# Kernel tuning notes

Measured on AMD Instinct MI355X. Metric: run time of the kernel, lower is better.

The kernel has to match this reference:

```python
import jax, jax.numpy as jnp
from jax import lax
import numpy as np

C = 16          # channels
K = 3           # deformable kernel size
PAD = 1


def conv3(x, w, b):
    # 3x3 SAME conv, NCHW / OIHW
    y = lax.conv_general_dilated(x, w, (1, 1), 'SAME',
                                 dimension_numbers=('NCHW', 'OIHW', 'NCHW'))
    return y + b[None, :, None, None]


def deform_conv2d(x, offsets, mask, w, b):
    """torchvision-style modulated deformable conv, stride=1, pad=1, dil=1.
    x: [B,C,H,W]; offsets: [B,2*K*K,H,W] (per-tap y,x interleaved);
    mask: [B,K*K,H,W]; w: [Cout,C,K,K]; b: [Cout]."""
    B, Cin, H, W = x.shape
    ky, kx = jnp.meshgrid(jnp.arange(K), jnp.arange(K), indexing='ij')
    ky = ky.reshape(-1).astype(x.dtype)   # [9]
    kx = kx.reshape(-1).astype(x.dtype)
    off = offsets.reshape(B, K * K, 2, H, W)  # off[:,k,0]=dy, off[:,k,1]=dx
    hh = jnp.arange(H, dtype=x.dtype)
    ww = jnp.arange(W, dtype=x.dtype)
    py = hh[None, None, :, None] + (ky - PAD)[None, :, None, None] + off[:, :, 0]  # [B,9,H,W]
    px = ww[None, None, None, :] + (kx - PAD)[None, :, None, None] + off[:, :, 1]
    y0 = jnp.floor(py)
    x0 = jnp.floor(px)
    dy = py - y0
    dx = px - x0

    def sample_one(img, y0b, x0b, dyb, dxb):
        # img [C,H,W]; y0b/x0b/dyb/dxb [9,H,W]
        y0i = y0b.astype(jnp.int32)
        x0i = x0b.astype(jnp.int32)

        def gather(yi, xi):
            valid = ((yi >= 0) & (yi < H) & (xi >= 0) & (xi < W)).astype(img.dtype)
            yc = jnp.clip(yi, 0, H - 1)
            xc = jnp.clip(xi, 0, W - 1)
            return img[:, yc, xc] * valid[None]   # [C,9,H,W]

        v00 = gather(y0i,     x0i)
        v01 = gather(y0i,     x0i + 1)
        v10 = gather(y0i + 1, x0i)
        v11 = gather(y0i + 1, x0i + 1)
        return (v00 * (1 - dyb) * (1 - dxb) + v01 * (1 - dyb) * dxb
                + v10 * dyb * (1 - dxb) + v11 * dyb * dxb)   # [C,9,H,W]

    sampled = jax.vmap(sample_one)(x, y0, x0, dy, dx)          # [B,C,9,H,W]
    sampled = sampled * mask[:, None]                           # modulate
    out = jnp.einsum('bckhw,ock->bohw', sampled, w.reshape(w.shape[0], Cin, K * K))
    return out + b[None, :, None, None]


def setup_inputs() -> dict:
    key = jax.random.key(0)
    ks = iter(jax.random.split(key, 32))

    def w(shape, scale=0.1):
        return (jax.random.normal(next(ks), shape, dtype=jnp.float32) * scale)

    B, H, W = 4, 256, 256
    d = {
        'f_E': jax.random.normal(next(ks), (B, C, H, W), dtype=jnp.float32),
        'f_F': jax.random.normal(next(ks), (B, C, H, W), dtype=jnp.float32),
        # SpatialAttentionBlock
        'sab_att_w1': w((C, 2 * C, 3, 3)), 'sab_att_b1': w((C,)),
        'sab_att_w2': w((1, C, 3, 3)),      'sab_att_b2': w((1,)),
        'sab_ref_w':  w((C, 2 * C, 3, 3)),  'sab_ref_b':  w((C,)),
        # DeformableConvLayer offset/mask net (last layer small -> modest offsets)
        'om_w1': w((C, 2 * C, 3, 3)),       'om_b1': w((C,)),
        'om_w2': w((C, C, 3, 3)),           'om_b2': w((C,)),
        'om_w3': w((3 * K * K, C, 3, 3), 0.05), 'om_b3': w((3 * K * K,), 0.05),
        # deformable conv weight/bias
        'dcb_w': w((C, C, 3, 3)),           'dcb_b': w((C,)),
        # refinements
        'dcbref_w': w((C, 2 * C, 3, 3)),    'dcbref_b': w((C,)),
        'fin_w':    w((C, 2 * C, 3, 3)),    'fin_b':    w((C,)),
    }
    return d


def reference(f_E, f_F,
              sab_att_w1, sab_att_b1, sab_att_w2, sab_att_b2,
              sab_ref_w, sab_ref_b,
              om_w1, om_b1, om_w2, om_b2, om_w3, om_b3,
              dcb_w, dcb_b, dcbref_w, dcbref_b, fin_w, fin_b):
    relu = jax.nn.relu
    # --- SAB branch: sab(f_E, f_F) ---
    comb = jnp.concatenate([f_E, f_F], axis=1)
    M_E = jax.nn.sigmoid(conv3(relu(conv3(comb, sab_att_w1, sab_att_b1)),
                               sab_att_w2, sab_att_b2))          # [B,1,H,W]
    f_Esa = f_E * M_E
    f_EFsa = relu(conv3(jnp.concatenate([f_Esa, f_F], axis=1), sab_ref_w, sab_ref_b))
    # --- DCB branch: dcb_layer(f_F, f_E) -> deform on f_E, cat([f_E, f_F]) ---
    comb2 = jnp.concatenate([f_E, f_F], axis=1)
    om = conv3(relu(conv3(relu(conv3(comb2, om_w1, om_b1)), om_w2, om_b2)),
               om_w3, om_b3)                                      # [B,27,H,W]
    offsets = om[:, :2 * K * K]
    mask = jax.nn.sigmoid(om[:, 2 * K * K:])
    f_Edc = relu(deform_conv2d(f_E, offsets, mask, dcb_w, dcb_b))
    f_EFdc = relu(conv3(jnp.concatenate([f_Edc, f_F], axis=1), dcbref_w, dcbref_b))
    # --- final fusion ---
    f_EF = relu(conv3(jnp.concatenate([f_EFsa, f_EFdc], axis=1), fin_w, fin_b))
    return f_EF
```

## Files before the change

### kernel.cpp

```cpp
#include <hip/hip_runtime.h>
#include <cstdint>
#include <cstddef>

#define HH 256
#define WW 256
#define HWW (HH * WW)

typedef __attribute__((ext_vector_type(8))) short bf16x8;
typedef __attribute__((ext_vector_type(4))) float f32x4;
typedef unsigned short ushort_t;

__device__ inline unsigned short f2bf(float f) {
  unsigned u = __float_as_uint(f);
  unsigned r = (u + 0x7fffu + ((u >> 16) & 1u)) >> 16;
  return (unsigned short)r;
}
__device__ inline float bf2f(unsigned short u) {
  return __uint_as_float((unsigned)u << 16);
}
__device__ inline float bf_lo(unsigned w) { return __uint_as_float(w << 16); }
__device__ inline float bf_hi(unsigned w) { return __uint_as_float(w & 0xffff0000u); }

struct RD { const float* src; void* dst; int cin, cout, mode; };
struct RA { RD d[9]; };

__global__ __launch_bounds__(256) void repack_k(RA a) {
  const RD t = a.d[blockIdx.x];
  if (t.mode == 2) {
    const int NST = (t.cin * 9 + 31) / 32;
    const int OT = (t.cout + 15) / 16;
    const int n = OT * NST * 512;
    unsigned short* dst = (unsigned short*)t.dst;
    for (int i = threadIdx.x; i < n; i += 256) {
      int j = i & 7;
      int l = (i >> 3) & 63;
      int rest = i >> 9;
      int s = rest % NST;
      int ot = rest / NST;
      int o = ot * 16 + (l & 15);
      int klin = s * 32 + ((l >> 4) << 3) + j;
      int tap = klin / t.cin;
      int c = klin % t.cin;
      float v = 0.f;
      if (tap < 9 && o < t.cout) v = t.src[(o * t.cin + c) * 9 + tap];
      dst[i] = f2bf(v);
    }
  } else {
    float* dst = (float*)t.dst;
    const int n = t.cin * t.cout * 9;
    for (int i = threadIdx.x; i < n; i += 256) {
      int k = i % 9;
      int rest = i / 9;
      int c = rest % t.cin;
      int o = rest / t.cin;
      if (t.mode == 0) dst[(c * 9 + k) * t.cout + o] = t.src[(o * t.cin + c) * 9 + k];
      else             dst[(k * t.cin + c) * t.cout + o] = t.src[(o * t.cin + c) * 9 + k];
    }
  }
}

__global__ __launch_bounds__(256) void nhwc2_k(
    const float* __restrict__ fe, const float* __restrict__ ff,
    unsigned short* __restrict__ xe, unsigned short* __restrict__ xf) {
  const int b = blockIdx.z;
  const int pixel = blockIdx.x * 256 + threadIdx.x;
#pragma unroll
  for (int t = 0; t < 2; ++t) {
    const float* src = t ? ff : fe;
    unsigned short* dst = t ? xf : xe;
    unsigned w[8];
#pragma unroll
    for (int j = 0; j < 8; ++j) {
      unsigned short lo = f2bf(src[((size_t)b * 16 + 2 * j) * HWW + pixel]);
      unsigned short hi = f2bf(src[((size_t)b * 16 + 2 * j + 1) * HWW + pixel]);
      w[j] = (unsigned)lo | ((unsigned)hi << 16);
    }
    uint4* d4 = (uint4*)(dst + ((size_t)b * HWW + pixel) * 16);
    d4[0] = make_uint4(w[0], w[1], w[2], w[3]);
    d4[1] = make_uint4(w[4], w[5], w[6], w[7]);
  }
}

template <int NSLOT, int OT, int OUT_MODE, int COUTR>
__global__ __launch_bounds__(256) void conv_nhwc(
    const unsigned short* __restrict__ inA, const unsigned short* __restrict__ inB,
    const unsigned short* __restrict__ wtm, const float* __restrict__ bias,
    void* __restrict__ outv) {
  constexpr int CIN = NSLOT * 8;
  constexpr int NST = (CIN * 9 + 31) / 32;
  constexpr int SHIFT = (NSLOT == 4) ? 1 : 2;
  constexpr int STRIDE = NSLOT * 16;
  constexpr int PX = 66, PY = 10;
  __shared__ __align__(16) char smem[PY * PX * STRIDE];

  const int b = blockIdx.z;
  const int tx0 = blockIdx.x * 64;
  const int ty0 = blockIdx.y * 8;
  const int tid = threadIdx.x;
  const int lane = tid & 63;
  const int wv = tid >> 6;

  bf16x8 afr[OT][NST];
#pragma unroll
  for (int ot = 0; ot < OT; ++ot)
#pragma unroll
    for (int s = 0; s < NST; ++s)
      afr[ot][s] = *(const bf16x8*)(wtm + (size_t)(((ot * NST + s) * 64 + lane) * 8));

  const int px_l = lane & 15;
  const int og = lane >> 4;

  f32x4 acc[8][OT];
#pragma unroll
  for (int ot = 0; ot < OT; ++ot) {
    f32x4 bv;
#pragma unroll
    for (int r = 0; r < 4; ++r) {
      int o = ot * 16 + og * 4 + r;
      bv[r] = bias[o < COUTR ? o : COUTR - 1];
    }
#pragma unroll
    for (int t = 0; t < 8; ++t) acc[t][ot] = bv;
  }

  for (int i = tid; i < PY * PX * NSLOT; i += 256) {
    int pp = i / NSLOT;
    int s = i - pp * NSLOT;
    int ly = pp / PX;
    int lx = pp - ly * PX;
    int gy = ty0 + ly - 1;
    int gx = tx0 + lx - 1;
    uint4 v = make_uint4(0, 0, 0, 0);
    if (gy >= 0 && gy < HH && gx >= 0 && gx < WW) {
      const unsigned short* src = (NSLOT == 2 || s < 2) ? inA : inB;
      int sl = (NSLOT == 4 && s >= 2) ? s - 2 : s;
      v = *(const uint4*)(src + ((size_t)b * HWW + (size_t)gy * WW + gx) * 16 + sl * 8);
    }
    int swz = (s ^ (pp >> SHIFT)) & (NSLOT - 1);
    *(uint4*)(smem + (size_t)pp * STRIDE + (swz << 4)) = v;
  }
  __syncthreads();

  int dpix[NST], dslot[NST];
#pragma unroll
  for (int s = 0; s < NST; ++s) {
    int klin = s * 32 + og * 8;
    int tap = klin / CIN;
    if (tap > 8) tap = 8;
    int coff = klin % CIN;
    dpix[s] = (tap / 3) * PX + (tap % 3);
    dslot[s] = coff >> 3;
  }

  const int oy_l = wv * 2;
#pragma unroll
  for (int t = 0; t < 8; ++t) {
    const int base_pix = (oy_l + (t >> 2)) * PX + (t & 3) * 16 + px_l;
#pragma unroll
    for (int s = 0; s < NST; ++s) {
      int pp = base_pix + dpix[s];
      int off = pp * STRIDE + (((dslot[s] ^ (pp >> SHIFT)) & (NSLOT - 1)) << 4);
      bf16x8 bvv = *(const bf16x8*)(smem + off);
#pragma unroll
      for (int ot = 0; ot < OT; ++ot)
        acc[t][ot] = __builtin_amdgcn_mfma_f32_16x16x32_bf16(afr[ot][s], bvv, acc[t][ot], 0, 0, 0);
    }
  }

#pragma unroll
  for (int t = 0; t < 8; ++t) {
    const int gy = ty0 + oy_l + (t >> 2);
    const int gx = tx0 + (t & 3) * 16 + px_l;
#pragma unroll
    for (int ot = 0; ot < OT; ++ot) {
      const int o0 = ot * 16 + og * 4;
      if (OUT_MODE == 2) {
        unsigned lo = (unsigned)f2bf(fmaxf(acc[t][ot][0], 0.f)) |
                      ((unsigned)f2bf(fmaxf(acc[t][ot][1], 0.f)) << 16);
        unsigned hi = (unsigned)f2bf(fmaxf(acc[t][ot][2], 0.f)) |
                      ((unsigned)f2bf(fmaxf(acc[t][ot][3], 0.f)) << 16);
        uint2* dst = (uint2*)((unsigned short*)outv +
                              ((size_t)b * HWW + (size_t)gy * WW + gx) * 16 + o0);
        *dst = make_uint2(lo, hi);
      } else if (OUT_MODE == 0) {
#pragma unroll
        for (int r = 0; r < 4; ++r) {
          int o = o0 + r;
          if (o < COUTR)
            ((float*)outv)[((size_t)b * COUTR + o) * HWW + (size_t)gy * WW + gx] =
                fmaxf(acc[t][ot][r], 0.f);
        }
      } else {
#pragma unroll
        for (int r = 0; r < 4; ++r) {
          int o = o0 + r;
          if (o < COUTR)
            ((unsigned short*)outv)[((size_t)b * COUTR + o) * HWW + (size_t)gy * WW + gx] =
                f2bf(acc[t][ot][r]);
        }
      }
    }
  }
}

__global__ __launch_bounds__(256) void gate_k(
    const unsigned short* __restrict__ xa, const unsigned short* __restrict__ xe,
    const float* __restrict__ wt, const float* __restrict__ bias,
    unsigned short* __restrict__ xsa) {
  const int b = blockIdx.z;
  const int y = blockIdx.x;
  const int x = threadIdx.x;
  float acc = bias[0];
#pragma unroll
  for (int ky = 0; ky < 3; ++ky) {
    int gy = y + ky - 1;
    if (gy < 0 || gy >= HH) continue;
#pragma unroll
    for (int kx = 0; kx < 3; ++kx) {
      int gx = x + kx - 1;
      if (gx < 0 || gx >= WW) continue;
      const int k = ky * 3 + kx;
      const uint4* p = (const uint4*)(xa + ((size_t)b * HWW + (size_t)gy * WW + gx) * 16);
      uint4 v0 = p[0], v1 = p[1];
      unsigned wv[8] = {v0.x, v0.y, v0.z, v0.w, v1.x, v1.y, v1.z, v1.w};
#pragma unroll
      for (int j = 0; j < 8; ++j) {
        acc = fmaf(bf_lo(wv[j]), wt[(2 * j) * 9 + k], acc);
        acc = fmaf(bf_hi(wv[j]), wt[(2 * j + 1) * 9 + k], acc);
      }
    }
  }
  float m = 1.0f / (1.0f + expf(-acc));
  const uint4* pe = (const uint4*)(xe + ((size_t)b * HWW + (size_t)y * WW + x) * 16);
  uint4 e0 = pe[0], e1 = pe[1];
  unsigned ev[8] = {e0.x, e0.y, e0.z, e0.w, e1.x, e1.y, e1.z, e1.w};
  unsigned r[8];
#pragma unroll
  for (int j = 0; j < 8; ++j) {
    unsigned short lo = f2bf(bf_lo(ev[j]) * m);
    unsigned short hi = f2bf(bf_hi(ev[j]) * m);
    r[j] = (unsigned)lo | ((unsigned)hi << 16);
  }
  uint4* d4 = (uint4*)(xsa + ((size_t)b * HWW + (size_t)y * WW + x) * 16);
  d4[0] = make_uint4(r[0], r[1], r[2], r[3]);
  d4[1] = make_uint4(r[4], r[5], r[6], r[7]);
}

__global__ __launch_bounds__(256) void deform_v4(
    const unsigned short* __restrict__ xn, const unsigned short* __restrict__ om,
    const float* __restrict__ wt, const float* __restrict__ bias,
    unsigned short* __restrict__ out) {
  const int bid = blockIdx.x;
  const int xcd = bid & 7;
  const int b = xcd >> 1;
  const int pb = ((bid >> 3) << 1) | (xcd & 1);
  const int pixel = pb * 256 + (int)threadIdx.x;
  const int y = pixel >> 8;
  const int xq = pixel & 255;
  const unsigned short* xb = xn + (size_t)b * HWW * 16;
  const unsigned short* omb = om + (size_t)b * 27 * HWW;

  float acc[16];
#pragma unroll
  for (int o = 0; o < 16; ++o) acc[o] = bias[o];

#pragma unroll
  for (int k = 0; k < 9; ++k) {
    float offy = bf2f(omb[(size_t)(2 * k) * HWW + pixel]);
    float offx = bf2f(omb[(size_t)(2 * k + 1) * HWW + pixel]);
    float m = 1.0f / (1.0f + expf(-bf2f(omb[(size_t)(18 + k) * HWW + pixel])));
    float py = (float)y + (float)(k / 3 - 1) + offy;
    float px = (float)xq + (float)(k % 3 - 1) + offx;
    float y0f = floorf(py);
    float x0f = floorf(px);
    float dy = py - y0f;
    float dx = px - x0f;
    int y0 = (int)y0f, x0 = (int)x0f;
    int y1 = y0 + 1, x1 = x0 + 1;
    bool vy0 = (y0 >= 0) && (y0 < HH);
    bool vy1 = (y1 >= 0) && (y1 < HH);
    bool vx0 = (x0 >= 0) && (x0 < WW);
    bool vx1 = (x1 >= 0) && (x1 < WW);
    int yc0 = min(max(y0, 0), HH - 1);
    int yc1 = min(max(y1, 0), HH - 1);
    int xc0 = min(max(x0, 0), WW - 1);
    int xc1 = min(max(x1, 0), WW - 1);
    float w00 = (1.f - dy) * (1.f - dx) * m;
    float w01 = (1.f - dy) * dx * m;
    float w10 = dy * (1.f - dx) * m;
    float w11 = dy * dx * m;
    if (!(vy0 && vx0)) w00 = 0.f;
    if (!(vy0 && vx1)) w01 = 0.f;
    if (!(vy1 && vx0)) w10 = 0.f;
    if (!(vy1 && vx1)) w11 = 0.f;

    const uint4* p00 = (const uint4*)(xb + (size_t)(yc0 * WW + xc0) * 16);
    const uint4* p01 = (const uint4*)(xb + (size_t)(yc0 * WW + xc1) * 16);
    const uint4* p10 = (const uint4*)(xb + (size_t)(yc1 * WW + xc0) * 16);
    const uint4* p11 = (const uint4*)(xb + (size_t)(yc1 * WW + xc1) * 16);
    uint4 a0 = p00[0], a1 = p00[1];
    uint4 b0 = p01[0], b1 = p01[1];
    uint4 c0 = p10[0], c1 = p10[1];
    uint4 d0 = p11[0], d1 = p11[1];
    unsigned wA[8] = {a0.x, a0.y, a0.z, a0.w, a1.x, a1.y, a1.z, a1.w};
    unsigned wB[8] = {b0.x, b0.y, b0.z, b0.w, b1.x, b1.y, b1.z, b1.w};
    unsigned wC[8] = {c0.x, c0.y, c0.z, c0.w, c1.x, c1.y, c1.z, c1.w};
    unsigned wD[8] = {d0.x, d0.y, d0.z, d0.w, d1.x, d1.y, d1.z, d1.w};

    float s[16];
#pragma unroll
    for (int j = 0; j < 8; ++j) {
      s[2 * j]     = bf_lo(wA[j]) * w00 + bf_lo(wB[j]) * w01 + bf_lo(wC[j]) * w10 + bf_lo(wD[j]) * w11;
      s[2 * j + 1] = bf_hi(wA[j]) * w00 + bf_hi(wB[j]) * w01 + bf_hi(wC[j]) * w10 + bf_hi(wD[j]) * w11;
    }
    const float* wk = wt + (size_t)k * 256;
#pragma unroll
    for (int c = 0; c < 16; ++c)
#pragma unroll
      for (int o = 0; o < 16; ++o)
        acc[o] = fmaf(s[c], wk[c * 16 + o], acc[o]);
  }
  unsigned r[8];
#pragma unroll
  for (int j = 0; j < 8; ++j) {
    unsigned short lo = f2bf(fmaxf(acc[2 * j], 0.f));
    unsigned short hi = f2bf(fmaxf(acc[2 * j + 1], 0.f));
    r[j] = (unsigned)lo | ((unsigned)hi << 16);
  }
  uint4* d4 = (uint4*)(out + ((size_t)b * HWW + pixel) * 16);
  d4[0] = make_uint4(r[0], r[1], r[2], r[3]);
  d4[1] = make_uint4(r[4], r[5], r[6], r[7]);
}

extern "C" void kernel_launch(void* const* d_in, const int* in_sizes, int n_in,
                              void* d_out, int out_size, void* d_ws, size_t ws_size,
                              hipStream_t stream) {
  (void)in_sizes; (void)n_in; (void)out_size; (void)ws_size;
  const float* f_E = (const float*)d_in[0];
  const float* f_F = (const float*)d_in[1];
  const float* att_w1 = (const float*)d_in[2];
  const float* att_b1 = (const float*)d_in[3];
  const float* att_w2 = (const float*)d_in[4];
  const float* att_b2 = (const float*)d_in[5];
  const float* ref_w = (const float*)d_in[6];
  const float* ref_b = (const float*)d_in[7];
  const float* om_w1 = (const float*)d_in[8];
  const float* om_b1 = (const float*)d_in[9];
  const float* om_w2 = (const float*)d_in[10];
  const float* om_b2 = (const float*)d_in[11];
  const float* om_w3 = (const float*)d_in[12];
  const float* om_b3 = (const float*)d_in[13];
  const float* dcb_w = (const float*)d_in[14];
  const float* dcb_b = (const float*)d_in[15];
  const float* dcbref_w = (const float*)d_in[16];
  const float* dcbref_b = (const float*)d_in[17];
  const float* fin_w = (const float*)d_in[18];
  const float* fin_b = (const float*)d_in[19];
  float* outp = (float*)d_out;

  const size_t TN = (size_t)4 * HWW * 16;
  unsigned short* XE  = (unsigned short*)d_ws;
  unsigned short* XF  = XE + TN;
  unsigned short* XA  = XF + TN;
  unsigned short* XSA = XA + TN;
  unsigned short* X2  = XSA + TN;
  unsigned short* XT  = X2 + TN;
  unsigned short* OMB = XT + TN;
  unsigned short* WM  = OMB + (size_t)4 * 27 * HWW;

  unsigned short* WM_att1 = WM;
  unsigned short* WM_ref  = WM_att1 + 4608;
  unsigned short* WM_om1  = WM_ref + 4608;
  unsigned short* WM_om2  = WM_om1 + 4608;
  unsigned short* WM_om3  = WM_om2 + 2560;
  unsigned short* WM_dref = WM_om3 + 5120;
  unsigned short* WM_fin  = WM_dref + 4608;
  float* WF_att2 = (float*)(WM_fin + 4608);
  float* WF_dcb  = WF_att2 + 144;

  RA ra;
  ra.d[0] = {att_w1, WM_att1, 32, 16, 2};
  ra.d[1] = {ref_w, WM_ref, 32, 16, 2};
  ra.d[2] = {om_w1, WM_om1, 32, 16, 2};
  ra.d[3] = {om_w2, WM_om2, 16, 16, 2};
  ra.d[4] = {om_w3, WM_om3, 16, 27, 2};
  ra.d[5] = {dcbref_w, WM_dref, 32, 16, 2};
  ra.d[6] = {fin_w, WM_fin, 32, 16, 2};
  ra.d[7] = {att_w2, WF_att2, 16, 1, 0};
  ra.d[8] = {dcb_w, WF_dcb, 16, 16, 1};
  repack_k<<<dim3(9), dim3(256), 0, stream>>>(ra);
  nhwc2_k<<<dim3(HWW / 256, 1, 4), dim3(256), 0, stream>>>(f_E, f_F, XE, XF);

  dim3 blk(256);
  dim3 gm(WW / 64, HH / 8, 4);

  conv_nhwc<4, 1, 2, 16><<<gm, blk, 0, stream>>>(XE, XF, WM_att1, att_b1, XA);
  gate_k<<<dim3(HH, 1, 4), blk, 0, stream>>>(XA, XE, WF_att2, att_b2, XSA);
  conv_nhwc<4, 1, 2, 16><<<gm, blk, 0, stream>>>(XSA, XF, WM_ref, ref_b, X2);
  conv_nhwc<4, 1, 2, 16><<<gm, blk, 0, stream>>>(XE, XF, WM_om1, om_b1, XT);
  conv_nhwc<2, 1, 2, 16><<<gm, blk, 0, stream>>>(XT, nullptr, WM_om2, om_b2, XA);
  conv_nhwc<2, 2, 1, 27><<<gm, blk, 0, stream>>>(XA, nullptr, WM_om3, om_b3, OMB);
  deform_v4<<<dim3(1024), blk, 0, stream>>>(XE, OMB, WF_dcb, dcb_b, XSA);
  conv_nhwc<4, 1, 2, 16><<<gm, blk, 0, stream>>>(XSA, XF, WM_dref, dcbref_b, XT);
  conv_nhwc<4, 1, 0, 16><<<gm, blk, 0, stream>>>(X2, XT, WM_fin, fin_b, outp);
}
```

Baseline: 128.8 us.

## Fuse sibling convs, gate into ref conv, and offset conv into deform

Merges the att1 and om1 convolutions, which read the same concatenated input, into one kernel that loads the tile once and issues MFMAs for both weight sets. Folds the sigmoid gate into the SAB refinement conv by recomputing the gate on the halo tile in shared memory. Computes the offset/mask conv inside the deformable kernel, keeping results in LDS so the 27-channel OMB buffer is never written to or read from HBM. This removes three launches and several full-tensor round trips, at the cost of recomputing halo gate values, higher register pressure, and a 2D-tiled deform layout that drops the XCD-aware block mapping.

```diff
diff --git a/kernel.cpp b/kernel.cpp
--- a/kernel.cpp
+++ b/kernel.cpp
@@ -8,7 +8,6 @@
 
 typedef __attribute__((ext_vector_type(8))) short bf16x8;
 typedef __attribute__((ext_vector_type(4))) float f32x4;
-typedef unsigned short ushort_t;
 
 __device__ inline unsigned short f2bf(float f) {
   unsigned u = __float_as_uint(f);
@@ -182,7 +181,7 @@
         uint2* dst = (uint2*)((unsigned short*)outv +
                               ((size_t)b * HWW + (size_t)gy * WW + gx) * 16 + o0);
         *dst = make_uint2(lo, hi);
-      } else if (OUT_MODE == 0) {
+      } else {
 #pragma unroll
         for (int r = 0; r < 4; ++r) {
           int o = o0 + r;
@@ -190,146 +189,421 @@
             ((float*)outv)[((size_t)b * COUTR + o) * HWW + (size_t)gy * WW + gx] =
                 fmaxf(acc[t][ot][r], 0.f);
         }
-      } else {
-#pragma unroll
-        for (int r = 0; r < 4; ++r) {
-          int o = o0 + r;
-          if (o < COUTR)
-            ((unsigned short*)outv)[((size_t)b * COUTR + o) * HWW + (size_t)gy * WW + gx] =
-                f2bf(acc[t][ot][r]);
+      }
+    }
+  }
+}
+
+__global__ __launch_bounds__(256) void conv_dual_k(
+    const unsigned short* __restrict__ inA, const unsigned short* __restrict__ inB,
+    const unsigned short* __restrict__ w1, const float* __restrict__ b1,
+    const unsigned short* __restrict__ w2, const float* __restrict__ b2,
+    unsigned short* __restrict__ out1, unsigned short* __restrict__ out2) {
+  constexpr int NSLOT = 4, NST = 9, SHIFT = 1, STRIDE = 64, PX = 66, PY = 10;
+  __shared__ __align__(16) char smem[PY * PX * STRIDE];
+
+  const int b = blockIdx.z;
+  const int tx0 = blockIdx.x * 64;
+  const int ty0 = blockIdx.y * 8;
+  const int tid = threadIdx.x;
+  const int lane = tid & 63;
+  const int wv = tid >> 6;
+
+  bf16x8 afr1[NST], afr2[NST];
+#pragma unroll
+  for (int s = 0; s < NST; ++s) {
+    afr1[s] = *(const bf16x8*)(w1 + (size_t)((s * 64 + lane) * 8));
+    afr2[s] = *(const bf16x8*)(w2 + (size_t)((s * 64 + lane) * 8));
+  }
+
+  const int px_l = lane & 15;
+  const int og = lane >> 4;
+
+  f32x4 acc1[8], acc2[8];
+  {
+    f32x4 bv1, bv2;
+#pragma unroll
+    for (int r = 0; r < 4; ++r) {
+      bv1[r] = b1[og * 4 + r];
+      bv2[r] = b2[og * 4 + r];
+    }
+#pragma unroll
+    for (int t = 0; t < 8; ++t) { acc1[t] = bv1; acc2[t] = bv2; }
+  }
+
+  for (int i = tid; i < PY * PX * NSLOT; i += 256) {
+    int pp = i / NSLOT;
+    int s = i - pp * NSLOT;
+    int ly = pp / PX;
+    int lx = pp - ly * PX;
+    int gy = ty0 + ly - 1;
+    int gx = tx0 + lx - 1;
+    uint4 v = make_uint4(0, 0, 0, 0);
+    if (gy >= 0 && gy < HH && gx >= 0 && gx < WW) {
+      const unsigned short* src = (s < 2) ? inA : inB;
+      int sl = (s >= 2) ? s - 2 : s;
+      v = *(const uint4*)(src + ((size_t)b * HWW + (size_t)gy * WW + gx) * 16 + sl * 8);
+    }
+    int swz = (s ^ (pp >> SHIFT)) & 3;
+    *(uint4*)(smem + (size_t)pp * STRIDE + (swz << 4)) = v;
+  }
+  __syncthreads();
+
+  int dpix[NST], dslot[NST];
+#pragma unroll
+  for (int s = 0; s < NST; ++s) {
+    int klin = s * 32 + og * 8;
+    int tap = klin / 32;
+    int coff = klin % 32;
+    dpix[s] = (tap / 3) * PX + (tap % 3);
+    dslot[s] = coff >> 3;
+  }
+
+  const int oy_l = wv * 2;
+#pragma unroll
+  for (int t = 0; t < 8; ++t) {
+    const int base_pix = (oy_l + (t >> 2)) * PX + (t & 3) * 16 + px_l;
+#pragma unroll
+    for (int s = 0; s < NST; ++s) {
+      int pp = base_pix + dpix[s];
+      int off = pp * STRIDE + (((dslot[s] ^ (pp >> SHIFT)) & 3) << 4);
+      bf16x8 bvv = *(const bf16x8*)(smem + off);
+      acc1[t] = __builtin_amdgcn_mfma_f32_16x16x32_bf16(afr1[s], bvv, acc1[t], 0, 0, 0);
+      acc2[t] = __builtin_amdgcn_mfma_f32_16x16x32_bf16(afr2[s], bvv, acc2[t], 0, 0, 0);
+    }
+  }
+
+#pragma unroll
+  for (int t = 0; t < 8; ++t) {
+    const int gy = ty0 + oy_l + (t >> 2);
+    const int gx = tx0 + (t & 3) * 16 + px_l;
+    const int o0 = og * 4;
+    size_t base = ((size_t)b * HWW + (size_t)gy * WW + gx) * 16 + o0;
+    {
+      unsigned lo = (unsigned)f2bf(fmaxf(acc1[t][0], 0.f)) |
+                    ((unsigned)f2bf(fmaxf(acc1[t][1], 0.f)) << 16);
+      unsigned hi = (unsigned)f2bf(fmaxf(acc1[t][2], 0.f)) |
+                    ((unsigned)f2bf(fmaxf(acc1[t][3], 0.f)) << 16);
+      *(uint2*)(out1 + base) = make_uint2(lo, hi);
+    }
+    {
+      unsigned lo = (unsigned)f2bf(fmaxf(acc2[t][0], 0.f)) |
+                    ((unsigned)f2bf(fmaxf(acc2[t][1], 0.f)) << 16);
+      unsigned hi = (unsigned)f2bf(fmaxf(acc2[t][2], 0.f)) |
+                    ((unsigned)f2bf(fmaxf(acc2[t][3], 0.f)) << 16);
+      *(uint2*)(out2 + base) = make_uint2(lo, hi);
+    }
+  }
+}
+
+__global__ __launch_bounds__(256) void sagate_k(
+    const unsigned short* __restrict__ xa, const unsigned short* __restrict__ xe,
+    const unsigned short* __restrict__ xf,
+    const float* __restrict__ gw, const float* __restrict__ gb,
+    const unsigned short* __restrict__ wtm, const float* __restrict__ bias,
+    unsigned short* __restrict__ out) {
+  constexpr int NSLOT = 4, NST = 9, SHIFT = 1, STRIDE = 64, PX = 66, PY = 10;
+  __shared__ __align__(16) char smem[PY * PX * STRIDE];
+
+  const int b = blockIdx.z;
+  const int tx0 = blockIdx.x * 64;
+  const int ty0 = blockIdx.y * 8;
+  const int tid = threadIdx.x;
+  const int lane = tid & 63;
+  const int wv = tid >> 6;
+
+  bf16x8 afr[NST];
+#pragma unroll
+  for (int s = 0; s < NST; ++s)
+    afr[s] = *(const bf16x8*)(wtm + (size_t)((s * 64 + lane) * 8));
+
+  const int px_l = lane & 15;
+  const int og = lane >> 4;
+
+  f32x4 acc[8];
+  {
+    f32x4 bv;
+#pragma unroll
+    for (int r = 0; r < 4; ++r) bv[r] = bias[og * 4 + r];
+#pragma unroll
+    for (int t = 0; t < 8; ++t) acc[t] = bv;
+  }
+
+  for (int i = tid; i < PY * PX * 2; i += 256) {
+    int pp = i >> 1;
+    int s = 2 + (i & 1);
+    int ly = pp / PX;
+    int lx = pp - ly * PX;
+    int gy = ty0 + ly - 1;
+    int gx = tx0 + lx - 1;
+    uint4 v = make_uint4(0, 0, 0, 0);
+    if (gy >= 0 && gy < HH && gx >= 0 && gx < WW)
+      v = *(const uint4*)(xf + ((size_t)b * HWW + (size_t)gy * WW + gx) * 16 + (s - 2) * 8);
+    int swz = (s ^ (pp >> SHIFT)) & 3;
+    *(uint4*)(smem + (size_t)pp * STRIDE + (swz << 4)) = v;
+  }
+
+  const float gbias = gb[0];
+  for (int i = tid; i < PY * PX; i += 256) {
+    int ly = i / PX;
+    int lx = i - ly * PX;
+    int gy = ty0 + ly - 1;
+    int gx = tx0 + lx - 1;
+    uint4 v0 = make_uint4(0, 0, 0, 0), v1 = make_uint4(0, 0, 0, 0);
+    if (gy >= 0 && gy < HH && gx >= 0 && gx < WW) {
+      float a = gbias;
+#pragma unroll
+      for (int ky = 0; ky < 3; ++ky) {
+        int ay = gy + ky - 1;
+        if (ay < 0 || ay >= HH) continue;
+#pragma unroll
+        for (int kx = 0; kx < 3; ++kx) {
+          int ax = gx + kx - 1;
+          if (ax < 0 || ax >= WW) continue;
+          const int k = ky * 3 + kx;
+          const uint4* p = (const uint4*)(xa + ((size_t)b * HWW + (size_t)ay * WW + ax) * 16);
+          uint4 t0 = p[0], t1 = p[1];
+          unsigned wv8[8] = {t0.x, t0.y, t0.z, t0.w, t1.x, t1.y, t1.z, t1.w};
+#pragma unroll
+          for (int j = 0; j < 8; ++j) {
+            a = fmaf(bf_lo(wv8[j]), gw[(2 * j) * 9 + k], a);
+            a = fmaf(bf_hi(wv8[j]), gw[(2 * j + 1) * 9 + k], a);
+          }
         }
       }
-    }
-  }
-}
-
-__global__ __launch_bounds__(256) void gate_k(
-    const unsigned short* __restrict__ xa, const unsigned short* __restrict__ xe,
-    const float* __restrict__ wt, const float* __restrict__ bias,
-    unsigned short* __restrict__ xsa) {
+      float m = 1.0f / (1.0f + expf(-a));
+      const uint4* pe = (const uint4*)(xe + ((size_t)b * HWW + (size_t)gy * WW + gx) * 16);
+      uint4 e0 = pe[0], e1 = pe[1];
+      unsigned ev[8] = {e0.x, e0.y, e0.z, e0.w, e1.x, e1.y, e1.z, e1.w};
+      unsigned r[8];
+#pragma unroll
+      for (int j = 0; j < 8; ++j) {
+        unsigned short lo = f2bf(bf_lo(ev[j]) * m);
+        unsigned short hi = f2bf(bf_hi(ev[j]) * m);
+        r[j] = (unsigned)lo | ((unsigned)hi << 16);
+      }
+      v0 = make_uint4(r[0], r[1], r[2], r[3]);
+      v1 = make_uint4(r[4], r[5], r[6], r[7]);
+    }
+    int swz0 = (0 ^ (i >> SHIFT)) & 3;
+    int swz1 = (1 ^ (i >> SHIFT)) & 3;
+    *(uint4*)(smem + (size_t)i * STRIDE + (swz0 << 4)) = v0;
+    *(uint4*)(smem + (size_t)i * STRIDE + (swz1 << 4)) = v1;
+  }
+  __syncthreads();
+
+  int dpix[NST], dslot[NST];
+#pragma unroll
+  for (int s = 0; s < NST; ++s) {
+    int klin = s * 32 + og * 8;
+    int tap = klin / 32;
+    int coff = klin % 32;
+    dpix[s] = (tap / 3) * PX + (tap % 3);
+    dslot[s] = coff >> 3;
+  }
+
+  const int oy_l = wv * 2;
+#pragma unroll
+  for (int t = 0; t < 8; ++t) {
+    const int base_pix = (oy_l + (t >> 2)) * PX + (t & 3) * 16 + px_l;
+#pragma unroll
+    for (int s = 0; s < NST; ++s) {
+      int pp = base_pix + dpix[s];
+      int off = pp * STRIDE + (((dslot[s] ^ (pp >> SHIFT)) & 3) << 4);
+      bf16x8 bvv = *(const bf16x8*)(smem + off);
+      acc[t] = __builtin_amdgcn_mfma_f32_16x16x32_bf16(afr[s], bvv, acc[t], 0, 0, 0);
+    }
+  }
+
+#pragma unroll
+  for (int t = 0; t < 8; ++t) {
+    const int gy = ty0 + oy_l + (t >> 2);
+    const int gx = tx0 + (t & 3) * 16 + px_l;
+    const int o0 = og * 4;
+    unsigned lo = (unsigned)f2bf(fmaxf(acc[t][0], 0.f)) |
+                  ((unsigned)f2bf(fmaxf(acc[t][1], 0.f)) << 16);
+    unsigned hi = (unsigned)f2bf(fmaxf(acc[t][2], 0.f)) |
+                  ((unsigned)f2bf(fmaxf(acc[t][3], 0.f)) << 16);
+    *(uint2*)(out + ((size_t)b * HWW + (size_t)gy * WW + gx) * 16 + o0) = make_uint2(lo, hi);
+  }
+}
+
+__global__ __launch_bounds__(256) void deform_fused_k(
+    const unsigned short* __restrict__ xa, const unsigned short* __restrict__ wtm,
+    const float* __restrict__ ob, const unsigned short* __restrict__ xe,
+    const float* __restrict__ dwt, const float* __restrict__ db,
+    unsigned short* __restrict__ out) {
+  constexpr int NSLOT = 2, NST = 5, OT = 2, SHIFT = 2, STRIDE = 32, PX = 66, PY = 10;
+  __shared__ __align__(16) char smem[8 * 64 * 36 * 2];
+  unsigned short* omld = (unsigned short*)smem;
+
   const int b = blockIdx.z;
-  const int y = blockIdx.x;
-  const int x = threadIdx.x;
-  float acc = bias[0];
-#pragma unroll
-  for (int ky = 0; ky < 3; ++ky) {
-    int gy = y + ky - 1;
-    if (gy < 0 || gy >= HH) continue;
-#pragma unroll
-    for (int kx = 0; kx < 3; ++kx) {
-      int gx = x + kx - 1;
-      if (gx < 0 || gx >= WW) continue;
-      const int k = ky * 3 + kx;
-      const uint4* p = (const uint4*)(xa + ((size_t)b * HWW + (size_t)gy * WW + gx) * 16);
-      uint4 v0 = p[0], v1 = p[1];
-      unsigned wv[8] = {v0.x, v0.y, v0.z, v0.w, v1.x, v1.y, v1.z, v1.w};
+  const int tx0 = blockIdx.x * 64;
+  const int ty0 = blockIdx.y * 8;
+  const int tid = threadIdx.x;
+  const int lane = tid & 63;
+  const int wv = tid >> 6;
+
+  bf16x8 afr[OT][NST];
+#pragma unroll
+  for (int ot = 0; ot < OT; ++ot)
+#pragma unroll
+    for (int s = 0; s < NST; ++s)
+      afr[ot][s] = *(const bf16x8*)(wtm + (size_t)(((ot * NST + s) * 64 + lane) * 8));
+
+  const int px_l = lane & 15;
+  const int og = lane >> 4;
+
+  f32x4 acc[8][OT];
+#pragma unroll
+  for (int ot = 0; ot < OT; ++ot) {
+    f32x4 bv;
+#pragma unroll
+    for (int r = 0; r < 4; ++r) {
+      int o = ot * 16 + og * 4 + r;
+      bv[r] = ob[o < 27 ? o : 26];
+    }
+#pragma unroll
+    for (int t = 0; t < 8; ++t) acc[t][ot] = bv;
+  }
+
+  for (int i = tid; i < PY * PX * NSLOT; i += 256) {
+    int pp = i >> 1;
+    int s = i & 1;
+    int ly = pp / PX;
+    int lx = pp - ly * PX;
+    int gy = ty0 + ly - 1;
+    int gx = tx0 + lx - 1;
+    uint4 v = make_uint4(0, 0, 0, 0);
+    if (gy >= 0 && gy < HH && gx >= 0 && gx < WW)
+      v = *(const uint4*)(xa + ((size_t)b * HWW + (size_t)gy * WW + gx) * 16 + s * 8);
+    int swz = (s ^ (pp >> SHIFT)) & 1;
+    *(uint4*)(smem + (size_t)pp * STRIDE + (swz << 4)) = v;
+  }
+  __syncthreads();
+
+  int dpix[NST], dslot[NST];
+#pragma unroll
+  for (int s = 0; s < NST; ++s) {
+    int klin = s * 32 + og * 8;
+    int tap = klin / 16;
+    if (tap > 8) tap = 8;
+    int coff = klin % 16;
+    dpix[s] = (tap / 3) * PX + (tap % 3);
+    dslot[s] = coff >> 3;
+  }
+
+  const int oy_l = wv * 2;
+#pragma unroll
+  for (int t = 0; t < 8; ++t) {
+    const int base_pix = (oy_l + (t >> 2)) * PX + (t & 3) * 16 + px_l;
+#pragma unroll
+    for (int s = 0; s < NST; ++s) {
+      int pp = base_pix + dpix[s];
+      int off = pp * STRIDE + (((dslot[s] ^ (pp >> SHIFT)) & 1) << 4);
+      bf16x8 bvv = *(const bf16x8*)(smem + off);
+#pragma unroll
+      for (int ot = 0; ot < OT; ++ot)
+        acc[t][ot] = __builtin_amdgcn_mfma_f32_16x16x32_bf16(afr[ot][s], bvv, acc[t][ot], 0, 0, 0);
+    }
+  }
+  __syncthreads();
+
+#pragma unroll
+  for (int t = 0; t < 8; ++t) {
+    const int pyl = oy_l + (t >> 2);
+    const int pxl = (t & 3) * 16 + px_l;
+#pragma unroll
+    for (int ot = 0; ot < OT; ++ot) {
+      const int o0 = ot * 16 + og * 4;
+      unsigned lo = (unsigned)f2bf(acc[t][ot][0]) | ((unsigned)f2bf(acc[t][ot][1]) << 16);
+      unsigned hi = (unsigned)f2bf(acc[t][ot][2]) | ((unsigned)f2bf(acc[t][ot][3]) << 16);
+      *(uint2*)(omld + (size_t)(pyl * 64 + pxl) * 36 + o0) = make_uint2(lo, hi);
+    }
+  }
+  __syncthreads();
+
+#pragma unroll
+  for (int half = 0; half < 2; ++half) {
+    const int p = tid + half * 256;
+    const int pyl = p >> 6;
+    const int pxl = p & 63;
+    const int gy = ty0 + pyl;
+    const int gx = tx0 + pxl;
+    const unsigned short* omp = omld + (size_t)(pyl * 64 + pxl) * 36;
+    const unsigned short* xb = xe + (size_t)b * HWW * 16;
+
+    float acc2[16];
+#pragma unroll
+    for (int o = 0; o < 16; ++o) acc2[o] = db[o];
+
+#pragma unroll
+    for (int k = 0; k < 9; ++k) {
+      float offy = bf2f(omp[2 * k]);
+      float offx = bf2f(omp[2 * k + 1]);
+      float m = 1.0f / (1.0f + expf(-bf2f(omp[18 + k])));
+      float py = (float)gy + (float)(k / 3 - 1) + offy;
+      float px = (float)gx + (float)(k % 3 - 1) + offx;
+      float y0f = floorf(py);
+      float x0f = floorf(px);
+      float dy = py - y0f;
+      float dx = px - x0f;
+      int y0 = (int)y0f, x0 = (int)x0f;
+      int y1 = y0 + 1, x1 = x0 + 1;
+      bool vy0 = (y0 >= 0) && (y0 < HH);
+      bool vy1 = (y1 >= 0) && (y1 < HH);
+      bool vx0 = (x0 >= 0) && (x0 < WW);
+      bool vx1 = (x1 >= 0) && (x1 < WW);
+      int yc0 = min(max(y0, 0), HH - 1);
+      int yc1 = min(max(y1, 0), HH - 1);
+      int xc0 = min(max(x0, 0), WW - 1);
+      int xc1 = min(max(x1, 0), WW - 1);
+      float w00 = (1.f - dy) * (1.f - dx) * m;
+      float w01 = (1.f - dy) * dx * m;
+      float w10 = dy * (1.f - dx) * m;
+      float w11 = dy * dx * m;
+      if (!(vy0 && vx0)) w00 = 0.f;
+      if (!(vy0 && vx1)) w01 = 0.f;
+      if (!(vy1 && vx0)) w10 = 0.f;
+      if (!(vy1 && vx1)) w11 = 0.f;
+
+      const uint4* p00 = (const uint4*)(xb + (size_t)(yc0 * WW + xc0) * 16);
+      const uint4* p01 = (const uint4*)(xb + (size_t)(yc0 * WW + xc1) * 16);
+      const uint4* p10 = (const uint4*)(xb + (size_t)(yc1 * WW + xc0) * 16);
+      const uint4* p11 = (const uint4*)(xb + (size_t)(yc1 * WW + xc1) * 16);
+      uint4 a0 = p00[0], a1 = p00[1];
+      uint4 b0 = p01[0], b1 = p01[1];
+      uint4 c0 = p10[0], c1 = p10[1];
+      uint4 d0 = p11[0], d1 = p11[1];
+      unsigned wA[8] = {a0.x, a0.y, a0.z, a0.w, a1.x, a1.y, a1.z, a1.w};
+      unsigned wB[8] = {b0.x, b0.y, b0.z, b0.w, b1.x, b1.y, b1.z, b1.w};
+      unsigned wC[8] = {c0.x, c0.y, c0.z, c0.w, c1.x, c1.y, c1.z, c1.w};
+      unsigned wD[8] = {d0.x, d0.y, d0.z, d0.w, d1.x, d1.y, d1.z, d1.w};
+
+      float sv[16];
 #pragma unroll
       for (int j = 0; j < 8; ++j) {
-        acc = fmaf(bf_lo(wv[j]), wt[(2 * j) * 9 + k], acc);
-        acc = fmaf(bf_hi(wv[j]), wt[(2 * j + 1) * 9 + k], acc);
+        sv[2 * j]     = bf_lo(wA[j]) * w00 + bf_lo(wB[j]) * w01 + bf_lo(wC[j]) * w10 + bf_lo(wD[j]) * w11;
+        sv[2 * j + 1] = bf_hi(wA[j]) * w00 + bf_hi(wB[j]) * w01 + bf_hi(wC[j]) * w10 + bf_hi(wD[j]) * w11;
       }
-    }
-  }
-  float m = 1.0f / (1.0f + expf(-acc));
-  const uint4* pe = (const uint4*)(xe + ((size_t)b * HWW + (size_t)y * WW + x) * 16);
-  uint4 e0 = pe[0], e1 = pe[1];
-  unsigned ev[8] = {e0.x, e0.y, e0.z, e0.w, e1.x, e1.y, e1.z, e1.w};
-  unsigned r[8];
-#pragma unroll
-  for (int j = 0; j < 8; ++j) {
-    unsigned short lo = f2bf(bf_lo(ev[j]) * m);
-    unsigned short hi = f2bf(bf_hi(ev[j]) * m);
-    r[j] = (unsigned)lo | ((unsigned)hi << 16);
-  }
-  uint4* d4 = (uint4*)(xsa + ((size_t)b * HWW + (size_t)y * WW + x) * 16);
-  d4[0] = make_uint4(r[0], r[1], r[2], r[3]);
-  d4[1] = make_uint4(r[4], r[5], r[6], r[7]);
-}
-
-__global__ __launch_bounds__(256) void deform_v4(
-    const unsigned short* __restrict__ xn, const unsigned short* __restrict__ om,
-    const float* __restrict__ wt, const float* __restrict__ bias,
-    unsigned short* __restrict__ out) {
-  const int bid = blockIdx.x;
-  const int xcd = bid & 7;
-  const int b = xcd >> 1;
-  const int pb = ((bid >> 3) << 1) | (xcd & 1);
-  const int pixel = pb * 256 + (int)threadIdx.x;
-  const int y = pixel >> 8;
-  const int xq = pixel & 255;
-  const unsigned short* xb = xn + (size_t)b * HWW * 16;
-  const unsigned short* omb = om + (size_t)b * 27 * HWW;
-
-  float acc[16];
-#pragma unroll
-  for (int o = 0; o < 16; ++o) acc[o] = bias[o];
-
-#pragma unroll
-  for (int k = 0; k < 9; ++k) {
-    float offy = bf2f(omb[(size_t)(2 * k) * HWW + pixel]);
-    float offx = bf2f(omb[(size_t)(2 * k + 1) * HWW + pixel]);
-    float m = 1.0f / (1.0f + expf(-bf2f(omb[(size_t)(18 + k) * HWW + pixel])));
-    float py = (float)y + (float)(k / 3 - 1) + offy;
-    float px = (float)xq + (float)(k % 3 - 1) + offx;
-    float y0f = floorf(py);
-    float x0f = floorf(px);
-    float dy = py - y0f;
-    float dx = px - x0f;
-    int y0 = (int)y0f, x0 = (int)x0f;
-    int y1 = y0 + 1, x1 = x0 + 1;
-    bool vy0 = (y0 >= 0) && (y0 < HH);
-    bool vy1 = (y1 >= 0) && (y1 < HH);
-    bool vx0 = (x0 >= 0) && (x0 < WW);
-    bool vx1 = (x1 >= 0) && (x1 < WW);
-    int yc0 = min(max(y0, 0), HH - 1);
-    int yc1 = min(max(y1, 0), HH - 1);
-    int xc0 = min(max(x0, 0), WW - 1);
-    int xc1 = min(max(x1, 0), WW - 1);
-    float w00 = (1.f - dy) * (1.f - dx) * m;
-    float w01 = (1.f - dy) * dx * m;
-    float w10 = dy * (1.f - dx) * m;
-    float w11 = dy * dx * m;
-    if (!(vy0 && vx0)) w00 = 0.f;
-    if (!(vy0 && vx1)) w01 = 0.f;
-    if (!(vy1 && vx0)) w10 = 0.f;
-    if (!(vy1 && vx1)) w11 = 0.f;
-
-    const uint4* p00 = (const uint4*)(xb + (size_t)(yc0 * WW + xc0) * 16);
-    const uint4* p01 = (const uint4*)(xb + (size_t)(yc0 * WW + xc1) * 16);
-    const uint4* p10 = (const uint4*)(xb + (size_t)(yc1 * WW + xc0) * 16);
-    const uint4* p11 = (const uint4*)(xb + (size_t)(yc1 * WW + xc1) * 16);
-    uint4 a0 = p00[0], a1 = p00[1];
-    uint4 b0 = p01[0], b1 = p01[1];
-    uint4 c0 = p10[0], c1 = p10[1];
-    uint4 d0 = p11[0], d1 = p11[1];
-    unsigned wA[8] = {a0.x, a0.y, a0.z, a0.w, a1.x, a1.y, a1.z, a1.w};
-    unsigned wB[8] = {b0.x, b0.y, b0.z, b0.w, b1.x, b1.y, b1.z, b1.w};
-    unsigned wC[8] = {c0.x, c0.y, c0.z, c0.w, c1.x, c1.y, c1.z, c1.w};
-    unsigned wD[8] = {d0.x, d0.y, d0.z, d0.w, d1.x, d1.y, d1.z, d1.w};
-
-    float s[16];
+      const float* wk = dwt + (size_t)k * 256;
+#pragma unroll
+      for (int c = 0; c < 16; ++c)
+#pragma unroll
+        for (int o = 0; o < 16; ++o)
+          acc2[o] = fmaf(sv[c], wk[c * 16 + o], acc2[o]);
+    }
+    unsigned r[8];
 #pragma unroll
     for (int j = 0; j < 8; ++j) {
-      s[2 * j]     = bf_lo(wA[j]) * w00 + bf_lo(wB[j]) * w01 + bf_lo(wC[j]) * w10 + bf_lo(wD[j]) * w11;
-      s[2 * j + 1] = bf_hi(wA[j]) * w00 + bf_hi(wB[j]) * w01 + bf_hi(wC[j]) * w10 + bf_hi(wD[j]) * w11;
-    }
-    const float* wk = wt + (size_t)k * 256;
-#pragma unroll
-    for (int c = 0; c < 16; ++c)
-#pragma unroll
-      for (int o = 0; o < 16; ++o)
-        acc[o] = fmaf(s[c], wk[c * 16 + o], acc[o]);
-  }
-  unsigned r[8];
-#pragma unroll
-  for (int j = 0; j < 8; ++j) {
-    unsigned short lo = f2bf(fmaxf(acc[2 * j], 0.f));
-    unsigned short hi = f2bf(fmaxf(acc[2 * j + 1], 0.f));
-    r[j] = (unsigned)lo | ((unsigned)hi << 16);
-  }
-  uint4* d4 = (uint4*)(out + ((size_t)b * HWW + pixel) * 16);
-  d4[0] = make_uint4(r[0], r[1], r[2], r[3]);
-  d4[1] = make_uint4(r[4], r[5], r[6], r[7]);
+      unsigned short lo = f2bf(fmaxf(acc2[2 * j], 0.f));
+      unsigned short hi = f2bf(fmaxf(acc2[2 * j + 1], 0.f));
+      r[j] = (unsigned)lo | ((unsigned)hi << 16);
+    }
+    uint4* d4 = (uint4*)(out + ((size_t)b * HWW + (size_t)gy * WW + gx) * 16);
+    d4[0] = make_uint4(r[0], r[1], r[2], r[3]);
+    d4[1] = make_uint4(r[4], r[5], r[6], r[7]);
+  }
 }
 
 extern "C" void kernel_launch(void* const* d_in, const int* in_sizes, int n_in,
@@ -362,11 +636,10 @@
   unsigned short* XE  = (unsigned short*)d_ws;
   unsigned short* XF  = XE + TN;
   unsigned short* XA  = XF + TN;
-  unsigned short* XSA = XA + TN;
-  unsigned short* X2  = XSA + TN;
-  unsigned short* XT  = X2 + TN;
-  unsigned short* OMB = XT + TN;
-  unsigned short* WM  = OMB + (size_t)4 * 27 * HWW;
+  unsigned short* XT  = XA + TN;
+  unsigned short* X2  = XT + TN;
+  unsigned short* XSA = X2 + TN;
+  unsigned short* WM  = XSA + TN;
 
   unsigned short* WM_att1 = WM;
   unsigned short* WM_ref  = WM_att1 + 4608;
@@ -394,13 +667,10 @@
   dim3 blk(256);
   dim3 gm(WW / 64, HH / 8, 4);
 
-  conv_nhwc<4, 1, 2, 16><<<gm, blk, 0, stream>>>(XE, XF, WM_att1, att_b1, XA);
-  gate_k<<<dim3(HH, 1, 4), blk, 0, stream>>>(XA, XE, WF_att2, att_b2, XSA);
-  conv_nhwc<4, 1, 2, 16><<<gm, blk, 0, stream>>>(XSA, XF, WM_ref, ref_b, X2);
-  conv_nhwc<4, 1, 2, 16><<<gm, blk, 0, stream>>>(XE, XF, WM_om1, om_b1, XT);
+  conv_dual_k<<<gm, blk, 0, stream>>>(XE, XF, WM_att1, att_b1, WM_om1, om_b1, XA, XT);
+  sagate_k<<<gm, blk, 0, stream>>>(XA, XE, XF, WF_att2, att_b2, WM_ref, ref_b, X2);
   conv_nhwc<2, 1, 2, 16><<<gm, blk, 0, stream>>>(XT, nullptr, WM_om2, om_b2, XA);
-  conv_nhwc<2, 2, 1, 27><<<gm, blk, 0, stream>>>(XA, nullptr, WM_om3, om_b3, OMB);
-  deform_v4<<<dim3(1024), blk, 0, stream>>>(XE, OMB, WF_dcb, dcb_b, XSA);
+  deform_fused_k<<<gm, blk, 0, stream>>>(XA, WM_om3, om_b3, XE, WF_dcb, dcb_b, XSA);
   conv_nhwc<4, 1, 2, 16><<<gm, blk, 0, stream>>>(XSA, XF, WM_dref, dcbref_b, XT);
   conv_nhwc<4, 1, 0, 16><<<gm, blk, 0, stream>>>(X2, XT, WM_fin, fin_b, outp);
 }
```

New measurement: 316.1 us. 145% more time.
